# Performance work log

Hardware: AMD Instinct MI355X
Metric: run time of the kernel (lower is better)

Reference implementation:

```python
import jax, jax.numpy as jnp
import numpy as np

B, F, T, Z, Y, X = 1, 8, 5, 16, 96, 96
N_RAYS = 32768   # n_rays_scan
K = 128          # n_points_ray
NEAR_PLANE = 0.01
C = F * Z        # conv channels after folding Z into channel dim


def setup_inputs() -> dict:
    key = jax.random.key(0)
    ks = jax.random.split(key, 6)
    vol = jax.random.normal(ks[0], (B, F, T, Z, Y, X), jnp.float32)
    # ray origins inside the normalized unit-cube scene
    rays_o = jax.random.uniform(ks[1], (T, N_RAYS, 3), jnp.float32, 0.1, 0.9)
    rd = jax.random.normal(ks[2], (T, N_RAYS, 3), jnp.float32)
    rays_d = rd / jnp.linalg.norm(rd, axis=-1, keepdims=True)
    conv_w = jax.random.normal(ks[3], (C, C, 3, 3, 3), jnp.float32) * (1.0 / np.sqrt(C * 27))
    conv_b = jnp.zeros((C,), jnp.float32)
    dens_w = jax.random.normal(ks[4], (F, 1), jnp.float32) * (1.0 / np.sqrt(F))
    dens_b = jnp.zeros((1,), jnp.float32)
    return dict(curr_feat_volume=vol, ray_start=rays_o, ray_direction=rays_d,
                conv_w=conv_w, conv_b=conv_b, dens_w=dens_w, dens_b=dens_b)


def _trilinear(vol, pts):
    """vol: [F,Z,Y,X]; pts: [...,3] with (x,y,z) in [0,1]. Returns [..., F]."""
    Fc, Zs, Ys, Xs = vol.shape
    gx = jnp.clip(pts[..., 0], 0.0, 1.0) * (Xs - 1)
    gy = jnp.clip(pts[..., 1], 0.0, 1.0) * (Ys - 1)
    gz = jnp.clip(pts[..., 2], 0.0, 1.0) * (Zs - 1)
    x0 = jnp.floor(gx).astype(jnp.int32); x1 = jnp.minimum(x0 + 1, Xs - 1)
    y0 = jnp.floor(gy).astype(jnp.int32); y1 = jnp.minimum(y0 + 1, Ys - 1)
    z0 = jnp.floor(gz).astype(jnp.int32); z1 = jnp.minimum(z0 + 1, Zs - 1)
    fx = gx - x0; fy = gy - y0; fz = gz - z0
    out = 0.0
    for zi, wz in ((z0, 1 - fz), (z1, fz)):
        for yi, wy in ((y0, 1 - fy), (y1, fy)):
            for xi, wx in ((x0, 1 - fx), (x1, fx)):
                out = out + vol[:, zi, yi, xi] * (wz * wy * wx)[None]
    return jnp.moveaxis(out, 0, -1)


def _render_t(vol_t, o, d, dens_w, dens_b):
    """One timestep: vol_t [F,Z,Y,X], o/d [N,3] -> depth [N,1]."""
    # SceneCollider: AABB [0,1]^3 with near_plane clamp
    t1 = (0.0 - o) / d
    t2 = (1.0 - o) / d
    near = jnp.max(jnp.minimum(t1, t2), axis=-1, keepdims=True)
    far = jnp.min(jnp.maximum(t1, t2), axis=-1, keepdims=True)
    near = jnp.maximum(near, NEAR_PLANE)
    far = jnp.maximum(far, near + 1e-6)
    # UniformSampler (deterministic bins)
    bins = jnp.linspace(0.0, 1.0, K + 1, dtype=jnp.float32)
    ts = near + bins[None, :] * (far - near)          # [N,K+1]
    starts = ts[:, :-1, None]                          # [N,K,1]
    ends = ts[:, 1:, None]
    mids = 0.5 * (starts + ends)
    pts = o[:, None, :] + d[:, None, :] * mids         # [N,K,3]
    # DensityField: trilinear feature gather + linear + softplus
    feats = _trilinear(vol_t, pts)                     # [N,K,F]
    density = jax.nn.softplus(feats @ dens_w + dens_b) # [N,K,1]
    # weights / transmittance (alpha compositing)
    deltas = ends - starts
    dd = density * deltas
    trans = jnp.exp(-jnp.concatenate([jnp.zeros_like(dd[:, :1]),
                                      jnp.cumsum(dd[:, :-1], axis=1)], axis=1))
    alpha = 1.0 - jnp.exp(-dd)
    weights = alpha * trans                            # [N,K,1]
    # DepthRenderer
    eps = 1e-10
    depth = jnp.sum(weights * starts, axis=-2) / (jnp.sum(weights, axis=-2) + eps)
    depth = jnp.clip(depth, starts.min(), starts.max())
    return depth                                       # [N,1]


def reference(curr_feat_volume, ray_start, ray_direction, conv_w, conv_b, dens_w, dens_b):
    # fold Z into channels and run dense Conv3d over (T,Y,X)
    x = jnp.transpose(curr_feat_volume, (0, 1, 3, 2, 4, 5)).reshape(B, F * Z, T, Y, X)
    y = jax.lax.conv_general_dilated(
        x, conv_w, window_strides=(1, 1, 1), padding='SAME',
        dimension_numbers=('NCDHW', 'OIDHW', 'NCDHW'))
    y = y + conv_b[None, :, None, None, None]
    future = jnp.transpose(y.reshape(B, F, Z, T, Y, X), (0, 3, 1, 2, 4, 5))  # [B,T,F,Z,Y,X]
    vols = future[0]                                   # [T,F,Z,Y,X]
    depth = jax.vmap(lambda v, o, d: _render_t(v, o, d, dens_w, dens_b))(
        vols, ray_start, ray_direction)                # [T,N,1]
    return depth
```

## Files before the change

kernel.cpp:

```cpp
#include <hip/hip_runtime.h>
#include <hip/hip_fp16.h>
#include <cstdint>
#include <cstddef>

#define T_DIM 5
#define F_DIM 8
#define Z_DIM 16
#define Y_DIM 96
#define X_DIM 96
#define NRAYS 32768
#define K_SAMP 128


struct __align__(16) Cell { __half2 h0, h1, h2, h3; };

typedef __attribute__((ext_vector_type(4))) float     f32x4;
typedef __attribute__((ext_vector_type(8))) _Float16  f16x8;

__device__ __forceinline__ float fexp2(float x) { return __builtin_amdgcn_exp2f(x); }
__device__ __forceinline__ float flog2(float x) { return __builtin_amdgcn_logf(x); }

__global__ __launch_bounds__(256) void setup_kernel(
        const float* __restrict__ xin, __half* __restrict__ inp,
        const float* __restrict__ w, const float* __restrict__ cb,
        const float* __restrict__ dw, __half* __restrict__ wB, float* __restrict__ bR,
        const float* __restrict__ ro, const float* __restrict__ rd,
        float* __restrict__ nearA, float* __restrict__ farA) {
    int b = blockIdx.x;
    if (b < 480) {
        __shared__ __half lds[96 * 136];
        int t = b / 96, y = b - (b / 96) * 96;
        for (int i = threadIdx.x; i < 12288; i += 256) {
            int row = i / 96;
            int x   = i - row * 96;
            int f = row >> 4, z = row & 15;
            float v = xin[(((size_t)(f * 5 + t) * 16 + z) * 96 + y) * 96 + x];
            lds[x * 136 + row] = __float2half(v);
        }
        __syncthreads();
        __half* ob = inp + ((size_t)(t * 96 + y) * 96) * 128;
        for (int c = threadIdx.x; c < 1536; c += 256) {
            int x = c >> 4, sub = c & 15;
            uint4 v = *(const uint4*)(lds + x * 136 + sub * 8);
            *(uint4*)(ob + (size_t)x * 128 + sub * 8) = v;
        }
    } else if (b < 696) {
        int i = (b - 480) * 256 + threadIdx.x;
        if (i < 16) {
            float s = 0.f;
            #pragma unroll
            for (int f = 0; f < 8; ++f) s += cb[f * 16 + i] * dw[f];
            bR[i] = s;
        }
        int cs  = i & 31;
        int zo  = (i >> 5) & 15;
        int pt  = i >> 9;
        int p   = pt / 27;
        int tap = pt - p * 27;
        int ci  = p * 32 + cs;
        float s = 0.f;
        #pragma unroll
        for (int f = 0; f < 8; ++f)
            s += w[(size_t)((f * 16 + zo) * 128 + ci) * 27 + tap] * dw[f];
        wB[i] = __float2half(s);
    } else {
        int gid = (b - 696) * 256 + threadIdx.x;
        const float* o = ro + (size_t)gid * 3;
        const float* d = rd + (size_t)gid * 3;
        float ox = o[0], oy = o[1], oz = o[2];
        float dx = d[0], dy = d[1], dz = d[2];
        float t1x = (0.f - ox) / dx, t2x = (1.f - ox) / dx;
        float t1y = (0.f - oy) / dy, t2y = (1.f - oy) / dy;
        float t1z = (0.f - oz) / dz, t2z = (1.f - oz) / dz;
        float nr = fmaxf(fmaxf(fminf(t1x, t2x), fminf(t1y, t2y)), fminf(t1z, t2z));
        float fr = fminf(fminf(fmaxf(t1x, t2x), fmaxf(t1y, t2y)), fmaxf(t1z, t2z));
        nr = fmaxf(nr, 0.01f);
        fr = fmaxf(fr, nr + 1e-6f);
        nearA[gid] = nr;
        farA[gid]  = fr;
    }
}

__global__ __launch_bounds__(128) void conv_mfma_kernel(
        const __half* __restrict__ inp, const __half* __restrict__ wB,
        float* __restrict__ part) {
    int bid = blockIdx.x;
    int wg  = (bid & 7) * 360 + (bid >> 3);
    int p   = wg & 3;
    int wq  = wg >> 2;
    int xs  = wq % 3;
    int rem = wq / 3;
    int yp  = rem % 48;
    int t   = rem / 48;
    int xseg = xs * 32, y0 = yp * 2;

    __shared__ __half lds[12 * 34 * 32];
    const int w    = threadIdx.x >> 6;
    const int lane = threadIdx.x & 63;
    const int l15  = lane & 15;
    const int ksub = lane >> 4;

    const int xl0 = threadIdx.x >> 2, sub0 = threadIdx.x & 3;
    const int xg0 = xseg + xl0 - 1;
    const bool xok0 = (unsigned)xg0 < 96u;
    const int glo0 = xg0 * 128 + sub0 * 8 + (p << 5);
    const int lof0 = xl0 * 32 + ((sub0 ^ ((xl0 >> 1) & 3)) << 3);
    const int q    = threadIdx.x / 12;
    const int rowh = threadIdx.x - q * 12;
    const int xl1  = 32 + (q >> 2), sub1 = q & 3;
    const int xg1  = xseg + xl1 - 1;
    const bool hwr = (q < 8);
    const bool hld = hwr && ((unsigned)xg1 < 96u);
    const int glo1 = xg1 * 128 + sub1 * 8 + (p << 5);
    const int lof1 = xl1 * 32 + ((sub1 ^ ((xl1 >> 1) & 3)) << 3);

    int offA[3];
    #pragma unroll
    for (int kx = 0; kx < 3; ++kx) {
        int X = l15 + kx;
        offA[kx] = X * 32 + ((ksub ^ ((X >> 1) & 3)) << 3);
    }

    uint4 vm[12];
    #pragma unroll
    for (int r = 0; r < 12; ++r) {
        int tt = t + (r >> 2) - 1;
        int yy = y0 + (r & 3) - 1;
        bool rok = ((unsigned)tt < 5u) & ((unsigned)yy < 96u);
        int rbase = (tt * 96 + yy) * 12288;
        uint4 v = {0u, 0u, 0u, 0u};
        if (rok & xok0) v = *(const uint4*)(inp + rbase + glo0);
        vm[r] = v;
    }
    uint4 vh = {0u, 0u, 0u, 0u};
    {
        int tt = t + (rowh >> 2) - 1;
        int yy = y0 + (rowh & 3) - 1;
        bool rok = ((unsigned)tt < 5u) & ((unsigned)yy < 96u);
        int rbase = (tt * 96 + yy) * 12288;
        if (rok & hld) vh = *(const uint4*)(inp + rbase + glo1);
    }
    #pragma unroll
    for (int r = 0; r < 12; ++r)
        *(uint4*)(lds + r * 1088 + lof0) = vm[r];
    if (hwr)
        *(uint4*)(lds + rowh * 1088 + lof1) = vh;
    __syncthreads();

    f32x4 acc0 = {0.f, 0.f, 0.f, 0.f};
    f32x4 acc1 = {0.f, 0.f, 0.f, 0.f};
    const __half* wp_base = wB + (size_t)p * 13824 + l15 * 32 + ksub * 8;
    #pragma unroll
    for (int kt = 0; kt < 3; ++kt) {
        #pragma unroll
        for (int ky = 0; ky < 3; ++ky) {
            const __half* lrow = lds + (kt * 4 + w + ky) * 1088;
            #pragma unroll
            for (int kx = 0; kx < 3; ++kx) {
                int tap = (kt * 3 + ky) * 3 + kx;
                f16x8 aw = *(const f16x8*)(wp_base + tap * 512);
                f16x8 b0 = *(const f16x8*)(lrow + offA[kx]);
                acc0 = __builtin_amdgcn_mfma_f32_16x16x32_f16(aw, b0, acc0, 0, 0, 0);
                f16x8 b1 = *(const f16x8*)(lrow + offA[kx] + 512);
                acc1 = __builtin_amdgcn_mfma_f32_16x16x32_f16(aw, b1, acc1, 0, 0, 0);
            }
        }
    }

    int yw = y0 + w;
    float* po = part + (size_t)p * 737280;
    #pragma unroll
    for (int r = 0; r < 4; ++r) {
        int zo = ksub * 4 + r;
        size_t o = (((size_t)t * 16 + zo) * 96 + yw) * 96 + xseg + l15;
        po[o]      = acc0[r];
        po[o + 16] = acc1[r];
    }
}

__global__ __launch_bounds__(256) void combine_kernel(
        const float* __restrict__ part, const float* __restrict__ bR,
        float* __restrict__ fld) {
    int i = blockIdx.x * 256 + threadIdx.x;
    if (i >= 184320) return;
    int z = (i / 2304) & 15;
    float b = bR[z];
    float4 r = make_float4(b, b, b, b);
    const float4* pp = (const float4*)part;
    #pragma unroll
    for (int s = 0; s < 4; ++s) {
        float4 a = pp[(size_t)s * 184320 + i];
        r.x += a.x; r.y += a.y; r.z += a.z; r.w += a.w;
    }
    ((float4*)fld)[i] = r;
}

__global__ __launch_bounds__(256) void pack_kernel(
        const float* __restrict__ fld, Cell* __restrict__ cellp) {
    int i = blockIdx.x * 256 + threadIdx.x;
    if (i >= 737280) return;
    int x = i % 96;
    int r = i / 96;
    int y = r % 96;
    int r2 = r / 96;
    int z = r2 % 16;
    int t = r2 / 16;
    const float* ft = fld + (size_t)t * 147456;
    int xp = min(x + 1, 95);
    int yr0 = y * 96, yr1 = min(y + 1, 95) * 96;
    int zr0 = z * 9216, zr1 = min(z + 1, 15) * 9216;
    float c000 = ft[zr0 + yr0 + x], c001 = ft[zr0 + yr0 + xp];
    float c010 = ft[zr0 + yr1 + x], c011 = ft[zr0 + yr1 + xp];
    float c100 = ft[zr1 + yr0 + x], c101 = ft[zr1 + yr0 + xp];
    float c110 = ft[zr1 + yr1 + x], c111 = ft[zr1 + yr1 + xp];
    Cell cl;
    cl.h0 = __floats2half2_rn(c000, c001 - c000);
    cl.h1 = __floats2half2_rn(c010, c011 - c010);
    cl.h2 = __floats2half2_rn(c100, c101 - c100);
    cl.h3 = __floats2half2_rn(c110, c111 - c110);
    cellp[i] = cl;
}

__global__ __launch_bounds__(256) void render_kernel(
        const float* __restrict__ ro, const float* __restrict__ rd,
        const Cell* __restrict__ cellp,
        const float* __restrict__ nearA, const float* __restrict__ farA,
        const float* __restrict__ dens_b, float* __restrict__ out) {
    int b = blockIdx.x;
    int b7 = b & 7, bhi = b >> 3;
    int t, seg;
    if (b7 < 5) { t = b7; seg = bhi; }
    else { int j = (b7 - 5) * 640 + bhi; t = j / 384; seg = 640 + j % 384; }
    int c = threadIdx.x & 7;
    int ray = t * NRAYS + seg * 32 + (threadIdx.x >> 3);

    const float* o = ro + (size_t)ray * 3;
    const float* d = rd + (size_t)ray * 3;
    float ox = o[0], oy = o[1], oz = o[2];
    float dx = d[0], dy = d[1], dz = d[2];
    float nr = nearA[ray], fr = farA[ray];
    const Cell* vt = cellp + (size_t)t * 147456;
    const float L2E = 1.4426950408889634f;
    float db2 = dens_b[0] * L2E;

    float span = fr - nr;
    float step = span * 0.0078125f;
    float s  = fmaf((float)(c * 16), step, nr);
    float mid = s + 0.5f * step;
    float pxg = fmaf(dx, mid, ox) * 95.f;
    float pyg = fmaf(dy, mid, oy) * 95.f;
    float pzg = fmaf(dz, mid, oz) * 15.f;
    float ddxg = dx * step * 95.f, ddyg = dy * step * 95.f, ddzg = dz * step * 15.f;

    float num = 0.f, den = 0.f, A2 = 0.f;
    float trans = 1.f;
    int pidx = -1;
    Cell cl;
    for (int kk = 0; kk < 16; ++kk) {
        int x0 = min(max((int)pxg, 0), 94);
        int y0 = min(max((int)pyg, 0), 94);
        int z0 = min(max((int)pzg, 0), 14);
        float fx = pxg - (float)x0, fy = pyg - (float)y0, fz = pzg - (float)z0;

        int idx = z0 * 9216 + y0 * 96 + x0;
        if (idx != pidx) {
            pidx = idx;
            cl = vt[idx];
        }

        float v00 = fmaf(fx, __half2float(__high2half(cl.h0)), __half2float(__low2half(cl.h0)));
        float v01 = fmaf(fx, __half2float(__high2half(cl.h1)), __half2float(__low2half(cl.h1)));
        float v10 = fmaf(fx, __half2float(__high2half(cl.h2)), __half2float(__low2half(cl.h2)));
        float v11 = fmaf(fx, __half2float(__high2half(cl.h3)), __half2float(__low2half(cl.h3)));
        float v0  = fmaf(fy, v01 - v00, v00);
        float v1  = fmaf(fy, v11 - v10, v10);
        float pre2 = fmaf(fmaf(fz, v1 - v0, v0), L2E, db2);

        float u = fexp2(-fabsf(pre2));
        float dens2 = fmaxf(pre2, 0.f) + flog2(1.f + u);
        float dd2 = dens2 * step;
        float ex = fexp2(-dd2);
        float wgt = (1.f - ex) * trans;
        num = fmaf(wgt, s, num);
        den += wgt;
        trans *= ex;
        A2 += dd2;
        s += step; pxg += ddxg; pyg += ddyg; pzg += ddzg;
    }
    int lane = threadIdx.x & 63;
    int qb = lane & ~7;
    float P = 0.f;
    #pragma unroll
    for (int j = 0; j < 7; ++j) {
        float Aj = __shfl(A2, qb + j, 64);
        P += (c > j) ? Aj : 0.f;
    }
    float sc = fexp2(-P);
    float numc = num * sc;
    float denc = den * sc;
    numc += __shfl_xor(numc, 1, 64);
    numc += __shfl_xor(numc, 2, 64);
    numc += __shfl_xor(numc, 4, 64);
    denc += __shfl_xor(denc, 1, 64);
    denc += __shfl_xor(denc, 2, 64);
    denc += __shfl_xor(denc, 4, 64);
    if (c == 0) {
        float depth = numc / (denc + 1e-10f);
        float slast = fmaf(0.9921875f, span, nr);
        depth = fminf(fmaxf(depth, nr), slast);
        out[ray] = depth;
    }
}

extern "C" void kernel_launch(void* const* d_in, const int* in_sizes, int n_in,
                              void* d_out, int out_size, void* d_ws, size_t ws_size,
                              hipStream_t stream) {
    const float* vol = (const float*)d_in[0];
    const float* ro  = (const float*)d_in[1];
    const float* rd  = (const float*)d_in[2];
    const float* cw  = (const float*)d_in[3];
    const float* cb  = (const float*)d_in[4];
    const float* dw  = (const float*)d_in[5];
    const float* dbp = (const float*)d_in[6];
    float* out = (float*)d_out;

    float* ws      = (float*)d_ws;
    float* fld     = ws;
    __half* inp    = (__half*)(ws + 737280);
    Cell*  cellp   = (Cell*)(ws + 737280);
    __half* wB     = (__half*)(ws + 737280 + 2949120);
    float* bR      = ws + 737280 + 2949120 + 27648;
    float* nearA   = bR + 32;
    float* farA    = nearA + 163840;
    float* part    = farA + 163840;

    hipLaunchKernelGGL(setup_kernel, dim3(1336), dim3(256), 0, stream,
                       vol, inp, cw, cb, dw, wB, bR, ro, rd, nearA, farA);
    hipLaunchKernelGGL(conv_mfma_kernel, dim3(2880), dim3(128), 0, stream,
                       inp, wB, part);
    hipLaunchKernelGGL(combine_kernel, dim3(720), dim3(256), 0, stream,
                       part, bR, fld);
    hipLaunchKernelGGL(pack_kernel, dim3(2880), dim3(256), 0, stream, fld, cellp);
    hipLaunchKernelGGL(render_kernel, dim3(5120), dim3(256), 0, stream,
                       ro, rd, cellp, nearA, farA, dbp, out);
}
```

Measured before the change: 161.0 us.

## Fuse partial-sum combine and cell packing into one shared-memory kernel

Merges the combine kernel, which sums the four split-K conv partials plus bias into a float field, with the pack kernel, which builds half-precision trilinear cells. Each block now loads a 9-row tile for two z planes into LDS and emits cells directly, so the intermediate field never makes a global round trip and one launch is dropped. In exchange, halo rows are summed redundantly (18 rows per 8 output rows) and a block-level sync is added.

```diff
diff --git a/kernel.cpp b/kernel.cpp
--- a/kernel.cpp
+++ b/kernel.cpp
@@ -178,47 +178,55 @@
     }
 }
 
-__global__ __launch_bounds__(256) void combine_kernel(
+__global__ __launch_bounds__(256) void combpack_kernel(
         const float* __restrict__ part, const float* __restrict__ bR,
-        float* __restrict__ fld) {
-    int i = blockIdx.x * 256 + threadIdx.x;
-    if (i >= 184320) return;
-    int z = (i / 2304) & 15;
-    float b = bR[z];
-    float4 r = make_float4(b, b, b, b);
+        Cell* __restrict__ cellp) {
+    int b = blockIdx.x;
+    int t = b / 192;
+    int r = b - t * 192;
+    int z = r / 12;
+    int y0 = (r - z * 12) * 8;
+    int z1 = min(z + 1, 15);
+
+    __shared__ float Lf[18 * 96];
     const float4* pp = (const float4*)part;
-    #pragma unroll
-    for (int s = 0; s < 4; ++s) {
-        float4 a = pp[(size_t)s * 184320 + i];
-        r.x += a.x; r.y += a.y; r.z += a.z; r.w += a.w;
-    }
-    ((float4*)fld)[i] = r;
-}
-
-__global__ __launch_bounds__(256) void pack_kernel(
-        const float* __restrict__ fld, Cell* __restrict__ cellp) {
-    int i = blockIdx.x * 256 + threadIdx.x;
-    if (i >= 737280) return;
-    int x = i % 96;
-    int r = i / 96;
-    int y = r % 96;
-    int r2 = r / 96;
-    int z = r2 % 16;
-    int t = r2 / 16;
-    const float* ft = fld + (size_t)t * 147456;
-    int xp = min(x + 1, 95);
-    int yr0 = y * 96, yr1 = min(y + 1, 95) * 96;
-    int zr0 = z * 9216, zr1 = min(z + 1, 15) * 9216;
-    float c000 = ft[zr0 + yr0 + x], c001 = ft[zr0 + yr0 + xp];
-    float c010 = ft[zr0 + yr1 + x], c011 = ft[zr0 + yr1 + xp];
-    float c100 = ft[zr1 + yr0 + x], c101 = ft[zr1 + yr0 + xp];
-    float c110 = ft[zr1 + yr1 + x], c111 = ft[zr1 + yr1 + xp];
-    Cell cl;
-    cl.h0 = __floats2half2_rn(c000, c001 - c000);
-    cl.h1 = __floats2half2_rn(c010, c011 - c010);
-    cl.h2 = __floats2half2_rn(c100, c101 - c100);
-    cl.h3 = __floats2half2_rn(c110, c111 - c110);
-    cellp[i] = cl;
+    for (int j = threadIdx.x; j < 432; j += 256) {
+        int row = j / 24, xq = j - row * 24;
+        int plane = row >= 9;
+        int zz = plane ? z1 : z;
+        int yy = min(y0 + row - (plane ? 9 : 0), 95);
+        size_t f4 = ((size_t)(t * 16 + zz) * 96 + yy) * 24 + xq;
+        float bz = bR[zz];
+        float4 a0 = pp[f4];
+        float4 a1 = pp[f4 + 184320];
+        float4 a2 = pp[f4 + 2 * 184320];
+        float4 a3 = pp[f4 + 3 * 184320];
+        float4 s;
+        s.x = bz + a0.x + a1.x + a2.x + a3.x;
+        s.y = bz + a0.y + a1.y + a2.y + a3.y;
+        s.z = bz + a0.z + a1.z + a2.z + a3.z;
+        s.w = bz + a0.w + a1.w + a2.w + a3.w;
+        *(float4*)(Lf + row * 96 + xq * 4) = s;
+    }
+    __syncthreads();
+
+    const size_t tz = (size_t)(t * 16 + z);
+    #pragma unroll
+    for (int k = 0; k < 3; ++k) {
+        int c = threadIdx.x + k * 256;
+        int yl = c / 96, x = c - yl * 96;
+        int xp = min(x + 1, 95);
+        float c000 = Lf[yl * 96 + x],        c001 = Lf[yl * 96 + xp];
+        float c010 = Lf[(yl + 1) * 96 + x],  c011 = Lf[(yl + 1) * 96 + xp];
+        float c100 = Lf[(9 + yl) * 96 + x],  c101 = Lf[(9 + yl) * 96 + xp];
+        float c110 = Lf[(10 + yl) * 96 + x], c111 = Lf[(10 + yl) * 96 + xp];
+        Cell cl;
+        cl.h0 = __floats2half2_rn(c000, c001 - c000);
+        cl.h1 = __floats2half2_rn(c010, c011 - c010);
+        cl.h2 = __floats2half2_rn(c100, c101 - c100);
+        cl.h3 = __floats2half2_rn(c110, c111 - c110);
+        cellp[(tz * 96 + y0 + yl) * 96 + x] = cl;
+    }
 }
 
 __global__ __launch_bounds__(256) void render_kernel(
@@ -325,7 +333,6 @@
     float* out = (float*)d_out;
 
     float* ws      = (float*)d_ws;
-    float* fld     = ws;
     __half* inp    = (__half*)(ws + 737280);
     Cell*  cellp   = (Cell*)(ws + 737280);
     __half* wB     = (__half*)(ws + 737280 + 2949120);
@@ -338,9 +345,8 @@
                        vol, inp, cw, cb, dw, wB, bR, ro, rd, nearA, farA);
     hipLaunchKernelGGL(conv_mfma_kernel, dim3(2880), dim3(128), 0, stream,
                        inp, wB, part);
-    hipLaunchKernelGGL(combine_kernel, dim3(720), dim3(256), 0, stream,
-                       part, bR, fld);
-    hipLaunchKernelGGL(pack_kernel, dim3(2880), dim3(256), 0, stream, fld, cellp);
+    hipLaunchKernelGGL(combpack_kernel, dim3(960), dim3(256), 0, stream,
+                       part, bR, cellp);
     hipLaunchKernelGGL(render_kernel, dim3(5120), dim3(256), 0, stream,
                        ro, rd, cellp, nearA, farA, dbp, out);
 }
```

After: 157.0 us. -2.5%, faster.
